# Kernel optimization log

Measured on AMD Instinct MI355X. Metric: run time of the kernel, lower is better.

The kernel has to match this reference:

```python
import jax, jax.numpy as jnp
import numpy as np

C64 = jnp.complex64


def _rx(theta):
    # RX(t) = [[cos(t/2), -i sin(t/2)], [-i sin(t/2), cos(t/2)]]; theta scalar or [B]
    h = 0.5 * theta
    c = jnp.cos(h).astype(C64)
    s = (-1j * jnp.sin(h)).astype(C64)
    return jnp.stack([jnp.stack([c, s], -1), jnp.stack([s, c], -1)], -2)


def _ry(theta):
    h = 0.5 * theta
    c = jnp.cos(h).astype(C64)
    s = jnp.sin(h).astype(C64)
    return jnp.stack([jnp.stack([c, -s], -1), jnp.stack([s, c], -1)], -2)


def _rz(theta):
    h = 0.5 * theta
    em = jnp.exp(-1j * h).astype(C64)
    ep = jnp.exp(1j * h).astype(C64)
    z = jnp.zeros_like(em)
    return jnp.stack([jnp.stack([em, z], -1), jnp.stack([z, ep], -1)], -2)


def _apply_1q(state, U, q):
    # state: [B, 2^Q] complex; wire 0 is the most significant bit.
    B = state.shape[0]
    s = state.reshape(B, 2 ** q, 2, -1)
    if U.ndim == 3:  # batched gate [B,2,2]
        s = jnp.einsum('bij,bajc->baic', U, s)
    else:  # shared gate [2,2]
        s = jnp.einsum('ij,bajc->baic', U, s)
    return s.reshape(B, -1)


def _cnot_adj(state, q):
    # CNOT with control q, target q+1 (adjacent wires)
    B = state.shape[0]
    s = state.reshape(B, 2 ** q, 2, 2, -1)
    s = s.at[:, :, 1].set(s[:, :, 1, ::-1])
    return s.reshape(B, -1)


def _pqc(context, W, b, pqc_params):
    Q = W.shape[0]
    L = pqc_params.shape[0]
    angles = jnp.pi * jnp.tanh(context @ W.T + b)  # [B, Q]
    B = angles.shape[0]
    state = jnp.zeros((B, 2 ** Q), C64).at[:, 0].set(1.0)
    # data-encoding RX layer (batch-dependent angles)
    for q in range(Q):
        state = _apply_1q(state, _rx(angles[:, q]), q)
    # variational layers
    for l in range(L):
        for q in range(Q):
            state = _apply_1q(state, _rx(pqc_params[l, q, 0]), q)
            state = _apply_1q(state, _ry(pqc_params[l, q, 1]), q)
            state = _apply_1q(state, _rz(pqc_params[l, q, 2]), q)
        for q in range(Q - 1):
            state = _cnot_adj(state, q)
    # <Z_q> expectation for every wire
    probs = state.real ** 2 + state.imag ** 2  # [B, 2^Q]
    p = probs.reshape((B,) + (2,) * Q)
    z = [p.sum(tuple(i + 1 for i in range(Q) if i != q)) for q in range(Q)]  # each [B,2]
    z = jnp.stack(z, -1)  # [B, 2, Q] -> wait: stack of [B,2] on -1 -> [B,2,Q]
    return z[:, 0, :] - z[:, 1, :]  # [B, Q]


def setup_inputs() -> dict:
    key = jax.random.key(0)
    k0, k1, k2, k3 = jax.random.split(key, 4)
    B, D, Q, L = 512, 256, 16, 4
    context = jax.random.normal(k0, (B, D), jnp.float32)
    W = jax.random.normal(k1, (Q, D), jnp.float32) / np.float32(np.sqrt(D))
    b = 0.01 * jax.random.normal(k2, (Q,), jnp.float32)
    pqc_params = 0.01 * jax.random.normal(k3, (L, Q, 3), jnp.float32)
    return {"context": context, "W": W, "b": b, "pqc_params": pqc_params}


def reference(context, W, b, pqc_params):
    return _pqc(context, W, b, pqc_params)
```

## Files before the change

kernel.cpp:

```cpp
#include <hip/hip_runtime.h>
#include <math.h>

#define NQ   16
#define NTH  256
#define NB   512

typedef float2 c32;

__device__ __forceinline__ c32 cmul(c32 a, c32 b) {
    return make_float2(a.x*b.x - a.y*b.y, a.x*b.y + a.y*b.x);
}
__device__ __forceinline__ c32 cfma_(c32 a, c32 b, c32 acc) {
    acc.x = fmaf(a.x, b.x, fmaf(-a.y, b.y, acc.x));
    acc.y = fmaf(a.x, b.y, fmaf( a.y, b.x, acc.y));
    return acc;
}
__device__ __forceinline__ c32 cfmaConjA(c32 a, c32 b, c32 acc) {
    acc.x = fmaf(a.x, b.x, fmaf( a.y, b.y, acc.x));
    acc.y = fmaf(a.x, b.y, fmaf(-a.y, b.x, acc.y));
    return acc;
}
__device__ __forceinline__ c32 cmulConjA(c32 a, c32 b) {
    return cfmaConjA(a, b, make_float2(0.f, 0.f));
}
__device__ __forceinline__ c32 conjc(c32 a){ return make_float2(a.x, -a.y); }
__device__ __forceinline__ c32 cadd(c32 a, c32 b){ return make_float2(a.x+b.x, a.y+b.y); }


__global__ __launch_bounds__(NTH, 2)
void pqc_mps_kernel(const float* __restrict__ ctx,
                    const float* __restrict__ Wm,
                    const float* __restrict__ bias,
                    const float* __restrict__ params,
                    float* __restrict__ out)
{
    __shared__ c32 Ac[14][272];
    __shared__ c32 A0c[16];
    __shared__ c32 A15v[32];
    __shared__ c32 Renv[15][144];
    __shared__ c32 Ssto[15][144];
    __shared__ c32 TRb[272];
    __shared__ c32 TLT[272];
    __shared__ c32 Lbuf[144];
    __shared__ c32 Ug[256];
    __shared__ c32 wv[64];
    __shared__ float angles[NQ];

    const int b = blockIdx.x;
    const int t = threadIdx.x;

    {
        const int q = t >> 4, g = t & 15;
        const float* crow = ctx + b * 256;
        const float* wrow = Wm + q * 256;
        float s = 0.f;
        #pragma unroll
        for (int j = 0; j < 16; ++j)
            s += crow[g + 16*j] * wrow[g + 16*j];
        #pragma unroll
        for (int m = 8; m; m >>= 1) s += __shfl_xor(s, m);
        if (g == 0) angles[q] = 3.14159265358979323846f * tanhf(s + bias[q]);
    }
    if (t < 64) {
        const float a  = params[t*3 + 0];
        const float bb = params[t*3 + 1];
        const float c  = params[t*3 + 2];
        const float ha = 0.5f*a, hb = 0.5f*bb, hc = 0.5f*c;
        const float ca = cosf(ha), sa = sinf(ha);
        const float cb = cosf(hb), sb = sinf(hb);
        const float cz = cosf(hc), sz = sinf(hc);
        const c32 m00 = make_float2( cb*ca,  sb*sa);
        const c32 m01 = make_float2(-sb*ca, -cb*sa);
        const c32 m10 = make_float2( sb*ca, -cb*sa);
        const c32 m11 = make_float2( cb*ca, -sb*sa);
        const c32 e0 = make_float2(cz, -sz);
        const c32 e1 = make_float2(cz,  sz);
        Ug[t*4 + 0] = cmul(e0, m00);
        Ug[t*4 + 1] = cmul(e0, m01);
        Ug[t*4 + 2] = cmul(e1, m10);
        Ug[t*4 + 3] = cmul(e1, m11);
    }
    __syncthreads();

    if (t < 64) {
        const int q = t >> 2, k = (t>>1)&1, i = t&1;
        const float h = 0.5f * angles[q];
        const float ch = cosf(h), sh = sinf(h);
        const int r0 = (i ^ k) << 1;
        const c32 u0 = Ug[(q<<2) + r0];
        const c32 u1 = Ug[(q<<2) + r0 + 1];
        wv[t] = make_float2(u0.x*ch + u1.y*sh, u0.y*ch - u1.x*sh);
    }
    __syncthreads();

    {
        const int r = t & 7, i = (t>>3)&1, a = t>>4;
        const int m0 = r&1, m1 = (r>>1)&1, m2 = r>>2;
        const int k0 = a&1, k1 = (a>>1)&1, k2 = (a>>2)&1, k3 = a>>3;
        #pragma unroll
        for (int q = 1; q <= 14; ++q) {
            const c32 u3 = Ug[((48+q)<<2) + ((i ^k3)<<1) + m2];
            const c32 u2 = Ug[((32+q)<<2) + ((m2^k2)<<1) + m1];
            const c32 u1 = Ug[((16+q)<<2) + ((m1^k1)<<1) + m0];
            const c32 ww = wv[(q<<2) + (k0<<1) + m0];
            Ac[q-1][a*17 + i*8 + r] = cmul(cmul(u3, u2), cmul(u1, ww));
        }
        if (t < 16) {
            const c32 u3 = Ug[(48<<2) + (i <<1) + m2];
            const c32 u2 = Ug[(32<<2) + (m2<<1) + m1];
            const c32 u1 = Ug[(16<<2) + (m1<<1) + m0];
            A0c[t] = cmul(cmul(u3, u2), cmul(u1, wv[m0]));
        }
        if (t >= 64 && t < 96) {
            const int idx = t - 64, aa = idx >> 1, ii = idx & 1;
            const int K0 = aa&1, K1 = (aa>>1)&1, K2 = (aa>>2)&1, K3 = aa>>3;
            c32 y1[2], y2[2];
            #pragma unroll
            for (int j1 = 0; j1 < 2; ++j1) {
                const int rr = (j1 ^ K1) << 1;
                y1[j1] = cfma_(Ug[((16+15)<<2)+rr], wv[60 + (K0<<1)],
                         cmul (Ug[((16+15)<<2)+rr+1], wv[60 + (K0<<1) + 1]));
            }
            #pragma unroll
            for (int j2 = 0; j2 < 2; ++j2) {
                const int rr = (j2 ^ K2) << 1;
                y2[j2] = cfma_(Ug[((32+15)<<2)+rr], y1[0],
                         cmul (Ug[((32+15)<<2)+rr+1], y1[1]));
            }
            const int rr = (ii ^ K3) << 1;
            A15v[(aa<<1)+ii] = cfma_(Ug[((48+15)<<2)+rr], y2[0],
                               cmul (Ug[((48+15)<<2)+rr+1], y2[1]));
        }
    }
    __syncthreads();

    const int bbR = t >> 3, iR = (t >> 2) & 1, gp0 = (t & 3) * 2;
    const int uL = t - 128;
    const int aL = uL >> 3, iL = (uL >> 2) & 1, bp0 = (uL & 3) * 2;
    const int mL = aL >> 3, alL = aL & 7;
    const int m2 = (t >> 6) & 1, bl2 = (t >> 3) & 7, bp2 = t & 7;
    const int i2L = uL >> 6;

    c32 aP1[8], sA0[8], sA1[8], pf2[16];

    if (t < 128) {
        const int m = t>>6, bl = (t>>3)&7, bp = t&7;
        c32 acc = cmulConjA(A15v[((m<<3)+bl)<<1],       A15v[((m<<3)+bp)<<1]);
        acc     = cfmaConjA(A15v[(((m<<3)+bl)<<1) + 1], A15v[(((m<<3)+bp)<<1) + 1], acc);
        Renv[14][m*72 + bl*9 + bp] = acc;
        const c32* Ap = Ac[13];
        #pragma unroll
        for (int g = 0; g < 8; ++g) aP1[g] = Ap[bbR*17 + iR*8 + g];
    } else {
        const int i = uL>>6, bl = (uL>>3)&7, bp = uL&7;
        const c32 sv = cmulConjA(A0c[(i<<3)+bl], A0c[(i<<3)+bp]);
        Ssto[0][i*72 + bl*9 + bp] = sv;
        Lbuf   [i*72 + bl*9 + bp] = sv;
        const c32* As = Ac[0];
        #pragma unroll
        for (int g = 0; g < 8; ++g) {
            sA0[g] = As[(mL*8+g)*17 + iL*8 + bp0];
            sA1[g] = As[(mL*8+g)*17 + iL*8 + bp0 + 1];
        }
    }
    __syncthreads();

    for (int s = 1; s <= 14; ++s) {
        const c32* Ap = Ac[14 - s];
        const c32* As = Ac[s - 1];

        if (t < 128) {
            const c32* RnB = Renv[15-s] + iR*72 + gp0*9;
            c32 x0 = make_float2(0.f,0.f), x1 = x0;
            #pragma unroll
            for (int g = 0; g < 8; ++g) {
                x0 = cfma_(aP1[g], RnB[g],   x0);
                x1 = cfma_(aP1[g], RnB[9+g], x1);
            }
            TRb[bbR*17 + iR*8 + gp0]     = conjc(x0);
            TRb[bbR*17 + iR*8 + gp0 + 1] = conjc(x1);
            #pragma unroll
            for (int k = 0; k < 16; ++k) pf2[k] = Ap[(m2*8+bp2)*17 + k];
        } else {
            const c32* Lr = Lbuf + mL*72 + alL*9;
            c32 x0 = make_float2(0.f,0.f), x1 = x0;
            #pragma unroll
            for (int g = 0; g < 8; ++g) {
                const c32 lv = Lr[g];
                x0 = cfma_(lv, sA0[g], x0);
                x1 = cfma_(lv, sA1[g], x1);
            }
            TLT[(iL*8 + bp0    )*17 + aL] = x0;
            TLT[(iL*8 + bp0 + 1)*17 + aL] = x1;
            #pragma unroll
            for (int k = 0; k < 16; ++k) pf2[k] = As[k*17 + i2L*8 + bl2];
        }
        __syncthreads();

        if (t < 128) {
            const c32* trR = TRb + (m2*8 + bl2)*17;
            c32 r0 = make_float2(0.f,0.f), r1 = r0;
            #pragma unroll
            for (int k = 0; k < 16; k += 2) {
                r0 = cfma_(trR[k],   pf2[k],   r0);
                r1 = cfma_(trR[k+1], pf2[k+1], r1);
            }
            Renv[14-s][m2*72 + bl2*9 + bp2] = cadd(r0, r1);
            if (s < 14) {
                const c32* ApN = Ac[13 - s];
                #pragma unroll
                for (int g = 0; g < 8; ++g) aP1[g] = ApN[bbR*17 + iR*8 + g];
            }
        } else {
            const c32* tlR = TLT + (i2L*8 + bp2)*17;
            c32 s0 = make_float2(0.f,0.f), s1 = s0;
            #pragma unroll
            for (int k = 0; k < 16; k += 2) {
                s0 = cfmaConjA(pf2[k],   tlR[k],   s0);
                s1 = cfmaConjA(pf2[k+1], tlR[k+1], s1);
            }
            const c32 sv = cadd(s0, s1);
            Ssto[s][i2L*72 + bl2*9 + bp2] = sv;
            Lbuf   [i2L*72 + bl2*9 + bp2] = sv;
            if (s < 14) {
                const c32* AsN = Ac[s];
                #pragma unroll
                for (int g = 0; g < 8; ++g) {
                    sA0[g] = AsN[(mL*8+g)*17 + iL*8 + bp0];
                    sA1[g] = AsN[(mL*8+g)*17 + iL*8 + bp0 + 1];
                }
            }
        }
        __syncthreads();
    }

    {
        const int q = t >> 4, g = t & 15;
        float val = 0.f;
        if (q < 15) {
            const int i = g>>3, bl = g&7;
            const float sign = i ? -1.f : 1.f;
            const c32* Sq = &Ssto[q][i*72 + bl*9];
            const c32* Rq = &Renv[q][i*72 + bl*9];
            #pragma unroll
            for (int j = 0; j < 8; ++j)
                val += sign * (Sq[j].x*Rq[j].x - Sq[j].y*Rq[j].y);
        } else {
            const int m = g>>3, al = g&7;
            const c32 a0 = A15v[((m*8+al)<<1) + 0];
            const c32 a1 = A15v[((m*8+al)<<1) + 1];
            #pragma unroll
            for (int j = 0; j < 8; ++j) {
                c32 d = cmulConjA(a0, A15v[((m*8+j)<<1) + 0]);
                const c32 d1 = cmulConjA(a1, A15v[((m*8+j)<<1) + 1]);
                d.x -= d1.x; d.y -= d1.y;
                const c32 Lv = Lbuf[m*72 + al*9 + j];
                val += Lv.x*d.x - Lv.y*d.y;
            }
        }
        #pragma unroll
        for (int mm = 8; mm; mm >>= 1) val += __shfl_xor(val, mm);
        if (g == 0) out[b*NQ + q] = val;
    }
}

extern "C" void kernel_launch(void* const* d_in, const int* in_sizes, int n_in,
                              void* d_out, int out_size, void* d_ws, size_t ws_size,
                              hipStream_t stream) {
    const float* ctx    = (const float*)d_in[0];
    const float* Wm     = (const float*)d_in[1];
    const float* bias   = (const float*)d_in[2];
    const float* params = (const float*)d_in[3];
    float* out = (float*)d_out;
    (void)in_sizes; (void)n_in; (void)out_size; (void)d_ws; (void)ws_size;
    pqc_mps_kernel<<<NB, NTH, 0, stream>>>(ctx, Wm, bias, params, out);
}
```

Measured before the change: 78.06 us.

## Split MPS tensor build into separate kernel writing global workspace

```diff
diff --git a/kernel.cpp b/kernel.cpp
--- a/kernel.cpp
+++ b/kernel.cpp
@@ -2,8 +2,12 @@
 #include <math.h>
 
 #define NQ   16
-#define NTH  256
 #define NB   512
+#define PI_F 3.14159265358979323846f
+#define BSTR 8192
+#define ATOF 4096
+#define A0OF 7680
+#define A15OF 7696
 
 typedef float2 c32;
 
@@ -26,42 +30,21 @@
 __device__ __forceinline__ c32 conjc(c32 a){ return make_float2(a.x, -a.y); }
 __device__ __forceinline__ c32 cadd(c32 a, c32 b){ return make_float2(a.x+b.x, a.y+b.y); }
 
-
-__global__ __launch_bounds__(NTH, 2)
-void pqc_mps_kernel(const float* __restrict__ ctx,
-                    const float* __restrict__ Wm,
-                    const float* __restrict__ bias,
-                    const float* __restrict__ params,
-                    float* __restrict__ out)
+__global__ __launch_bounds__(64)
+void pqc_build_kernel(const float* __restrict__ ctx,
+                      const float* __restrict__ Wm,
+                      const float* __restrict__ bias,
+                      const float* __restrict__ params,
+                      c32* __restrict__ ws)
 {
-    __shared__ c32 Ac[14][272];
-    __shared__ c32 A0c[16];
-    __shared__ c32 A15v[32];
-    __shared__ c32 Renv[15][144];
-    __shared__ c32 Ssto[15][144];
-    __shared__ c32 TRb[272];
-    __shared__ c32 TLT[272];
-    __shared__ c32 Lbuf[144];
     __shared__ c32 Ug[256];
-    __shared__ c32 wv[64];
-    __shared__ float angles[NQ];
+    __shared__ c32 fq[32];
 
     const int b = blockIdx.x;
     const int t = threadIdx.x;
 
+    c32 u00,u01,u10,u11;
     {
-        const int q = t >> 4, g = t & 15;
-        const float* crow = ctx + b * 256;
-        const float* wrow = Wm + q * 256;
-        float s = 0.f;
-        #pragma unroll
-        for (int j = 0; j < 16; ++j)
-            s += crow[g + 16*j] * wrow[g + 16*j];
-        #pragma unroll
-        for (int m = 8; m; m >>= 1) s += __shfl_xor(s, m);
-        if (g == 0) angles[q] = 3.14159265358979323846f * tanhf(s + bias[q]);
-    }
-    if (t < 64) {
         const float a  = params[t*3 + 0];
         const float bb = params[t*3 + 1];
         const float c  = params[t*3 + 2];
@@ -75,99 +58,138 @@
         const c32 m11 = make_float2( cb*ca, -sb*sa);
         const c32 e0 = make_float2(cz, -sz);
         const c32 e1 = make_float2(cz,  sz);
-        Ug[t*4 + 0] = cmul(e0, m00);
-        Ug[t*4 + 1] = cmul(e0, m01);
-        Ug[t*4 + 2] = cmul(e1, m10);
-        Ug[t*4 + 3] = cmul(e1, m11);
+        u00 = cmul(e0, m00); u01 = cmul(e0, m01);
+        u10 = cmul(e1, m10); u11 = cmul(e1, m11);
+        Ug[t*4+0]=u00; Ug[t*4+1]=u01; Ug[t*4+2]=u10; Ug[t*4+3]=u11;
+    }
+    {
+        const int q = t & 15, seg = t >> 4;
+        const float4* c4 = (const float4*)(ctx + (size_t)b*256);
+        const float4* w4 = (const float4*)(Wm  + (size_t)q*256);
+        float s = 0.f;
+        #pragma unroll
+        for (int j = 0; j < 16; ++j) {
+            const float4 x = c4[seg*16 + j], y = w4[seg*16 + j];
+            s = fmaf(x.x,y.x, fmaf(x.y,y.y, fmaf(x.z,y.z, fmaf(x.w,y.w, s))));
+        }
+        s += __shfl_xor(s, 16);
+        s += __shfl_xor(s, 32);
+        if (seg == 0) {
+            const float ang = PI_F * tanhf(s + bias[q]);
+            const float h = 0.5f*ang, ch = cosf(h), sh = sinf(h);
+            fq[q*2+0] = make_float2(u00.x*ch + u01.y*sh, u00.y*ch - u01.x*sh);
+            fq[q*2+1] = make_float2(u10.x*ch + u11.y*sh, u10.y*ch - u11.x*sh);
+        }
     }
     __syncthreads();
 
-    if (t < 64) {
-        const int q = t >> 2, k = (t>>1)&1, i = t&1;
-        const float h = 0.5f * angles[q];
-        const float ch = cosf(h), sh = sinf(h);
-        const int r0 = (i ^ k) << 1;
-        const c32 u0 = Ug[(q<<2) + r0];
-        const c32 u1 = Ug[(q<<2) + r0 + 1];
-        wv[t] = make_float2(u0.x*ch + u1.y*sh, u0.y*ch - u1.x*sh);
-    }
-    __syncthreads();
-
-    {
-        const int r = t & 7, i = (t>>3)&1, a = t>>4;
-        const int m0 = r&1, m1 = (r>>1)&1, m2 = r>>2;
-        const int k0 = a&1, k1 = (a>>1)&1, k2 = (a>>2)&1, k3 = a>>3;
-        #pragma unroll
-        for (int q = 1; q <= 14; ++q) {
-            const c32 u3 = Ug[((48+q)<<2) + ((i ^k3)<<1) + m2];
-            const c32 u2 = Ug[((32+q)<<2) + ((m2^k2)<<1) + m1];
-            const c32 u1 = Ug[((16+q)<<2) + ((m1^k1)<<1) + m0];
-            const c32 ww = wv[(q<<2) + (k0<<1) + m0];
-            Ac[q-1][a*17 + i*8 + r] = cmul(cmul(u3, u2), cmul(u1, ww));
-        }
-        if (t < 16) {
-            const c32 u3 = Ug[(48<<2) + (i <<1) + m2];
-            const c32 u2 = Ug[(32<<2) + (m2<<1) + m1];
-            const c32 u1 = Ug[(16<<2) + (m1<<1) + m0];
-            A0c[t] = cmul(cmul(u3, u2), cmul(u1, wv[m0]));
-        }
-        if (t >= 64 && t < 96) {
-            const int idx = t - 64, aa = idx >> 1, ii = idx & 1;
-            const int K0 = aa&1, K1 = (aa>>1)&1, K2 = (aa>>2)&1, K3 = aa>>3;
-            c32 y1[2], y2[2];
-            #pragma unroll
-            for (int j1 = 0; j1 < 2; ++j1) {
-                const int rr = (j1 ^ K1) << 1;
-                y1[j1] = cfma_(Ug[((16+15)<<2)+rr], wv[60 + (K0<<1)],
-                         cmul (Ug[((16+15)<<2)+rr+1], wv[60 + (K0<<1) + 1]));
-            }
-            #pragma unroll
-            for (int j2 = 0; j2 < 2; ++j2) {
-                const int rr = (j2 ^ K2) << 1;
-                y2[j2] = cfma_(Ug[((32+15)<<2)+rr], y1[0],
-                         cmul (Ug[((32+15)<<2)+rr+1], y1[1]));
-            }
-            const int rr = (ii ^ K3) << 1;
-            A15v[(aa<<1)+ii] = cfma_(Ug[((48+15)<<2)+rr], y2[0],
-                               cmul (Ug[((48+15)<<2)+rr+1], y2[1]));
-        }
-    }
-    __syncthreads();
+    c32* W = ws + (size_t)b * BSTR;
+    for (int q = 1; q <= 14; ++q) {
+        const int base = (q-1)*256;
+        #pragma unroll
+        for (int rep = 0; rep < 4; ++rep) {
+            const int idx = rep*64 + t;
+            {
+                const int a = idx>>4, i = (idx>>3)&1, r = idx&7;
+                const int m0=r&1, m1=(r>>1)&1, m2=r>>2;
+                const int k0=a&1, k1=(a>>1)&1, k2=(a>>2)&1, k3=a>>3;
+                const c32 u3 = Ug[((48+q)<<2) + ((i ^k3)<<1) + m2];
+                const c32 u2 = Ug[((32+q)<<2) + ((m2^k2)<<1) + m1];
+                const c32 u1 = Ug[((16+q)<<2) + ((m1^k1)<<1) + m0];
+                W[base + idx] = cmul(cmul(u3,u2), cmul(u1, fq[2*q + (k0^m0)]));
+            }
+            {
+                const int a = idx&15, ir = idx>>4;
+                const int i = ir>>3, r = ir&7;
+                const int m0=r&1, m1=(r>>1)&1, m2=r>>2;
+                const int k0=a&1, k1=(a>>1)&1, k2=(a>>2)&1, k3=a>>3;
+                const c32 u3 = Ug[((48+q)<<2) + ((i ^k3)<<1) + m2];
+                const c32 u2 = Ug[((32+q)<<2) + ((m2^k2)<<1) + m1];
+                const c32 u1 = Ug[((16+q)<<2) + ((m1^k1)<<1) + m0];
+                W[ATOF + base + idx] = cmul(cmul(u3,u2), cmul(u1, fq[2*q + (k0^m0)]));
+            }
+        }
+    }
+    if (t < 16) {
+        const int i = t>>3, r = t&7;
+        const int m0=r&1, m1=(r>>1)&1, m2=r>>2;
+        const c32 u3 = Ug[(48<<2) + (i <<1) + m2];
+        const c32 u2 = Ug[(32<<2) + (m2<<1) + m1];
+        const c32 u1 = Ug[(16<<2) + (m1<<1) + m0];
+        W[A0OF + t] = cmul(cmul(u3,u2), cmul(u1, fq[m0]));
+    }
+    if (t >= 32 && t < 64) {
+        const int idx = t-32, aa = idx>>1, ii = idx&1;
+        const int K0=aa&1, K1=(aa>>1)&1, K2=(aa>>2)&1, K3=aa>>3;
+        c32 y1[2], y2[2];
+        #pragma unroll
+        for (int j1 = 0; j1 < 2; ++j1) {
+            const int rr = (j1 ^ K1) << 1;
+            y1[j1] = cfma_(Ug[((16+15)<<2)+rr], fq[30 + K0],
+                     cmul (Ug[((16+15)<<2)+rr+1], fq[30 + (K0^1)]));
+        }
+        #pragma unroll
+        for (int j2 = 0; j2 < 2; ++j2) {
+            const int rr = (j2 ^ K2) << 1;
+            y2[j2] = cfma_(Ug[((32+15)<<2)+rr], y1[0],
+                     cmul (Ug[((32+15)<<2)+rr+1], y1[1]));
+        }
+        const int rr = (ii ^ K3) << 1;
+        W[A15OF + (aa<<1) + ii] = cfma_(Ug[((48+15)<<2)+rr], y2[0],
+                                  cmul (Ug[((48+15)<<2)+rr+1], y2[1]));
+    }
+}
+
+__global__ __launch_bounds__(256, 4)
+void pqc_sweep_kernel(const c32* __restrict__ ws, float* __restrict__ out)
+{
+    __shared__ c32 Renv[15][144];
+    __shared__ c32 Ssto[15][144];
+    __shared__ c32 TRb[272];
+    __shared__ c32 TLT[272];
+    __shared__ c32 Lbuf[144];
+
+    const int b = blockIdx.x;
+    const int t = threadIdx.x;
+    const c32* Ab  = ws + (size_t)b * BSTR;
+    const c32* ATb = Ab + ATOF;
+    const c32* A0  = Ab + A0OF;
+    const c32* A15 = Ab + A15OF;
 
     const int bbR = t >> 3, iR = (t >> 2) & 1, gp0 = (t & 3) * 2;
-    const int uL = t - 128;
-    const int aL = uL >> 3, iL = (uL >> 2) & 1, bp0 = (uL & 3) * 2;
-    const int mL = aL >> 3, alL = aL & 7;
-    const int m2 = (t >> 6) & 1, bl2 = (t >> 3) & 7, bp2 = t & 7;
+    const int uL  = t - 128;
+    const int aL  = uL >> 3, iL = (uL >> 2) & 1, bp0 = (uL & 3) * 2;
+    const int mL  = aL >> 3, alL = aL & 7;
+    const int m2  = (t >> 6) & 1, bl2 = (t >> 3) & 7, bp2 = t & 7;
     const int i2L = uL >> 6;
 
     c32 aP1[8], sA0[8], sA1[8], pf2[16];
 
     if (t < 128) {
         const int m = t>>6, bl = (t>>3)&7, bp = t&7;
-        c32 acc = cmulConjA(A15v[((m<<3)+bl)<<1],       A15v[((m<<3)+bp)<<1]);
-        acc     = cfmaConjA(A15v[(((m<<3)+bl)<<1) + 1], A15v[(((m<<3)+bp)<<1) + 1], acc);
+        c32 acc = cmulConjA(A15[((m<<3)+bl)<<1],       A15[((m<<3)+bp)<<1]);
+        acc     = cfmaConjA(A15[(((m<<3)+bl)<<1) + 1], A15[(((m<<3)+bp)<<1) + 1], acc);
         Renv[14][m*72 + bl*9 + bp] = acc;
-        const c32* Ap = Ac[13];
-        #pragma unroll
-        for (int g = 0; g < 8; ++g) aP1[g] = Ap[bbR*17 + iR*8 + g];
+        const c32* Ap = Ab + 13*256;
+        #pragma unroll
+        for (int g = 0; g < 8; ++g) aP1[g] = Ap[bbR*16 + iR*8 + g];
     } else {
         const int i = uL>>6, bl = (uL>>3)&7, bp = uL&7;
-        const c32 sv = cmulConjA(A0c[(i<<3)+bl], A0c[(i<<3)+bp]);
+        const c32 sv = cmulConjA(A0[(i<<3)+bl], A0[(i<<3)+bp]);
         Ssto[0][i*72 + bl*9 + bp] = sv;
         Lbuf   [i*72 + bl*9 + bp] = sv;
-        const c32* As = Ac[0];
+        const c32* AsT = ATb;
         #pragma unroll
         for (int g = 0; g < 8; ++g) {
-            sA0[g] = As[(mL*8+g)*17 + iL*8 + bp0];
-            sA1[g] = As[(mL*8+g)*17 + iL*8 + bp0 + 1];
+            sA0[g] = AsT[(iL*8 + bp0    )*16 + mL*8 + g];
+            sA1[g] = AsT[(iL*8 + bp0 + 1)*16 + mL*8 + g];
         }
     }
     __syncthreads();
 
     for (int s = 1; s <= 14; ++s) {
-        const c32* Ap = Ac[14 - s];
-        const c32* As = Ac[s - 1];
+        const c32* Ap  = Ab  + (14 - s)*256;
+        const c32* AsT = ATb + (s - 1)*256;
 
         if (t < 128) {
             const c32* RnB = Renv[15-s] + iR*72 + gp0*9;
@@ -180,7 +202,7 @@
             TRb[bbR*17 + iR*8 + gp0]     = conjc(x0);
             TRb[bbR*17 + iR*8 + gp0 + 1] = conjc(x1);
             #pragma unroll
-            for (int k = 0; k < 16; ++k) pf2[k] = Ap[(m2*8+bp2)*17 + k];
+            for (int k = 0; k < 16; ++k) pf2[k] = Ap[(m2*8+bp2)*16 + k];
         } else {
             const c32* Lr = Lbuf + mL*72 + alL*9;
             c32 x0 = make_float2(0.f,0.f), x1 = x0;
@@ -193,7 +215,7 @@
             TLT[(iL*8 + bp0    )*17 + aL] = x0;
             TLT[(iL*8 + bp0 + 1)*17 + aL] = x1;
             #pragma unroll
-            for (int k = 0; k < 16; ++k) pf2[k] = As[k*17 + i2L*8 + bl2];
+            for (int k = 0; k < 16; ++k) pf2[k] = AsT[(i2L*8+bl2)*16 + k];
         }
         __syncthreads();
 
@@ -207,9 +229,9 @@
             }
             Renv[14-s][m2*72 + bl2*9 + bp2] = cadd(r0, r1);
             if (s < 14) {
-                const c32* ApN = Ac[13 - s];
+                const c32* ApN = Ab + (13 - s)*256;
                 #pragma unroll
-                for (int g = 0; g < 8; ++g) aP1[g] = ApN[bbR*17 + iR*8 + g];
+                for (int g = 0; g < 8; ++g) aP1[g] = ApN[bbR*16 + iR*8 + g];
             }
         } else {
             const c32* tlR = TLT + (i2L*8 + bp2)*17;
@@ -223,11 +245,11 @@
             Ssto[s][i2L*72 + bl2*9 + bp2] = sv;
             Lbuf   [i2L*72 + bl2*9 + bp2] = sv;
             if (s < 14) {
-                const c32* AsN = Ac[s];
+                const c32* AsN = ATb + s*256;
                 #pragma unroll
                 for (int g = 0; g < 8; ++g) {
-                    sA0[g] = AsN[(mL*8+g)*17 + iL*8 + bp0];
-                    sA1[g] = AsN[(mL*8+g)*17 + iL*8 + bp0 + 1];
+                    sA0[g] = AsN[(iL*8 + bp0    )*16 + mL*8 + g];
+                    sA1[g] = AsN[(iL*8 + bp0 + 1)*16 + mL*8 + g];
                 }
             }
         }
@@ -247,12 +269,12 @@
                 val += sign * (Sq[j].x*Rq[j].x - Sq[j].y*Rq[j].y);
         } else {
             const int m = g>>3, al = g&7;
-            const c32 a0 = A15v[((m*8+al)<<1) + 0];
-            const c32 a1 = A15v[((m*8+al)<<1) + 1];
+            const c32 a0 = A15[((m*8+al)<<1) + 0];
+            const c32 a1 = A15[((m*8+al)<<1) + 1];
             #pragma unroll
             for (int j = 0; j < 8; ++j) {
-                c32 d = cmulConjA(a0, A15v[((m*8+j)<<1) + 0]);
-                const c32 d1 = cmulConjA(a1, A15v[((m*8+j)<<1) + 1]);
+                c32 d = cmulConjA(a0, A15[((m*8+j)<<1) + 0]);
+                const c32 d1 = cmulConjA(a1, A15[((m*8+j)<<1) + 1]);
                 d.x -= d1.x; d.y -= d1.y;
                 const c32 Lv = Lbuf[m*72 + al*9 + j];
                 val += Lv.x*d.x - Lv.y*d.y;
@@ -272,6 +294,8 @@
     const float* bias   = (const float*)d_in[2];
     const float* params = (const float*)d_in[3];
     float* out = (float*)d_out;
-    (void)in_sizes; (void)n_in; (void)out_size; (void)d_ws; (void)ws_size;
-    pqc_mps_kernel<<<NB, NTH, 0, stream>>>(ctx, Wm, bias, params, out);
-}
+    c32* ws = (c32*)d_ws;
+    (void)in_sizes; (void)n_in; (void)out_size; (void)ws_size;
+    pqc_build_kernel<<<NB, 64, 0, stream>>>(ctx, Wm, bias, params, ws);
+    pqc_sweep_kernel<<<NB, 256, 0, stream>>>(ws, out);
+}
```

Result: slower. 116.9 us (+49.7%).
